# Optimization experiments

Hardware: AMD Instinct MI355X
Metric: run time of the kernel (lower is better)

## Reference

```python
import jax, jax.numpy as jnp
import numpy as np

B, T, N, Fi, Hh, K = 8, 24, 4096, 64, 128, 2
C = Fi + Hh  # concat channel dim


def _uniform(k, shape, fan_in):
    b = 1.0 / np.sqrt(fan_in)
    return jax.random.uniform(k, shape, jnp.float32, -b, b)


def setup_inputs() -> dict:
    key = jax.random.key(0)
    ks = jax.random.split(key, 7)
    x = jax.random.normal(ks[0], (B, T, N, Fi), jnp.float32)
    # torch Conv2d default init: U(-1/sqrt(fan_in), 1/sqrt(fan_in)), fan_in = C_in*kh*kw
    gate_w = _uniform(ks[1], (2 * Hh, C, K, 1), C * K)
    gate_b = _uniform(ks[2], (2 * Hh,), C * K)
    cand_w = _uniform(ks[3], (Hh, C, K, 1), C * K)
    cand_b = _uniform(ks[4], (Hh,), C * K)
    out_w = _uniform(ks[5], (Fi, Hh, 1, 1), Hh)
    out_b = _uniform(ks[6], (Fi,), Hh)
    return {"x": x, "gate_w": gate_w, "gate_b": gate_b,
            "cand_w": cand_w, "cand_b": cand_b,
            "out_w": out_w, "out_b": out_b}


def reference(x, gate_w, gate_b, cand_w, cand_b, out_w, out_b):
    # Conv2d with kernel (K,1), padding (K-1,0) on a height-1 input, keeping only
    # output row 0: out[0] = W[:, :, K-1] @ in[0] (+ zero-padded rows). So each
    # conv reduces to a per-node channel matmul with kernel row K-1.
    Wg = gate_w[:, :, K - 1, 0]  # [2H, C]
    Wc = cand_w[:, :, K - 1, 0]  # [H, C]
    Wo = out_w[:, :, 0, 0]       # [Fi, H]

    def step(h, x_t):
        # h: [B, H, N], x_t: [B, N, Fi]
        xt = jnp.swapaxes(x_t, 1, 2)                       # [B, Fi, N]
        inp = jnp.concatenate([xt, h], axis=1)             # [B, C, N]
        gates = jnp.einsum('bcn,oc->bon', inp, Wg) + gate_b[None, :, None]
        r, z = jnp.split(jax.nn.sigmoid(gates), 2, axis=1)  # each [B, H, N]
        cinp = jnp.concatenate([xt, r * h], axis=1)        # [B, C, N]
        h_tilde = jnp.tanh(jnp.einsum('bcn,oc->bon', cinp, Wc) + cand_b[None, :, None])
        h_t = (1.0 - z) * h + z * h_tilde
        return h_t, h_t

    h0 = jnp.zeros((B, Hh, N), x.dtype)
    _, hs = jax.lax.scan(step, h0, jnp.swapaxes(x, 0, 1))  # hs: [T, B, H, N]
    h_stack = jnp.transpose(hs, (1, 2, 0, 3))              # [B, H, T, N]
    out = jnp.einsum('bhtn,oh->botn', h_stack, Wo) + out_b[None, :, None, None]
    return jax.nn.relu(jnp.transpose(out, (0, 2, 3, 1)))   # [B, T, N, Fi]
```

## Files before the change

kernel.cpp:

```cpp
#include <hip/hip_runtime.h>

#define B_ 8
#define T_ 24
#define N_ 4096
#define FI 64
#define HH 128
#define CC 192
#define COLS 64
#define SI 200
#define SC 136

typedef __bf16 bf16_t;
typedef bf16_t bf16x8 __attribute__((ext_vector_type(8)));
typedef bf16_t bf16x4 __attribute__((ext_vector_type(4)));
typedef float  f32x4  __attribute__((ext_vector_type(4)));

static __device__ __forceinline__ f32x4 mfma16(bf16x8 a, bf16x8 b, f32x4 c) {
    return __builtin_amdgcn_mfma_f32_16x16x32_bf16(a, b, c, 0, 0, 0);
}

__global__ __launch_bounds__(512, 2) void mgru_kernel(
    const float* __restrict__ x,
    const float* __restrict__ gate_w,
    const float* __restrict__ gate_b,
    const float* __restrict__ cand_w,
    const float* __restrict__ cand_b,
    const float* __restrict__ out_w,
    const float* __restrict__ out_b,
    float* __restrict__ out)
{
    __shared__ __align__(16) bf16_t inpT[COLS * SI];
    __shared__ __align__(16) bf16_t cinpT[COLS * SC];

    const int tid  = threadIdx.x;
    const int wave = tid >> 6;
    const int lane = tid & 63;
    const int quad = lane >> 4;
    const int l16  = lane & 15;

    const int bb = blockIdx.x >> 6;
    const int n0 = (blockIdx.x & 63) * COLS;

    for (int i = tid; i < COLS * HH; i += 512) {
        const int col = i >> 7, ch = i & (HH - 1);
        inpT[col * SI + FI + ch] = (bf16_t)0.0f;
    }

    bf16x8 gA[2][6];
    #pragma unroll
    for (int p = 0; p < 2; ++p) {
        const int m = p * 128 + wave * 16 + l16;
        #pragma unroll
        for (int kt = 0; kt < 6; ++kt) {
            bf16x8 f;
            #pragma unroll
            for (int j = 0; j < 8; ++j)
                f[j] = (bf16_t)gate_w[(m * CC + kt * 32 + quad * 8 + j) * 2 + 1];
            gA[p][kt] = f;
        }
    }
    bf16x8 cA[6];
    {
        const int m = wave * 16 + l16;
        #pragma unroll
        for (int kt = 0; kt < 6; ++kt) {
            bf16x8 f;
            #pragma unroll
            for (int j = 0; j < 8; ++j)
                f[j] = (bf16_t)cand_w[(m * CC + kt * 32 + quad * 8 + j) * 2 + 1];
            cA[kt] = f;
        }
    }
    bf16x8 oA[4];
    {
        const int m = (wave >> 1) * 16 + l16;
        #pragma unroll
        for (int kt = 0; kt < 4; ++kt) {
            bf16x8 f;
            #pragma unroll
            for (int j = 0; j < 8; ++j)
                f[j] = (bf16_t)out_w[m * HH + kt * 32 + quad * 8 + j];
            oA[kt] = f;
        }
    }

    f32x4 gBr, gBz, cB, oB;
    #pragma unroll
    for (int r = 0; r < 4; ++r) {
        gBr[r] = gate_b[wave * 16 + quad * 4 + r];
        gBz[r] = gate_b[128 + wave * 16 + quad * 4 + r];
        cB[r]  = cand_b[wave * 16 + quad * 4 + r];
        oB[r]  = out_b[(wave >> 1) * 16 + quad * 4 + r];
    }

    f32x4 hreg[4];
    #pragma unroll
    for (int nt = 0; nt < 4; ++nt) hreg[nt] = f32x4{0.f, 0.f, 0.f, 0.f};

    const int xcol = tid >> 3;
    const int xcg  = (tid & 7) * 8;
    const float* xbase = x   + ((size_t)bb * T_ * N_ + n0) * FI;
    float*       obase = out + ((size_t)bb * T_ * N_ + n0) * FI;

    f32x4 p0 = *(const f32x4*)(xbase + xcol * FI + xcg);
    f32x4 p1 = *(const f32x4*)(xbase + xcol * FI + xcg + 4);

    for (int t = 0; t < T_; ++t) {
        {
            bf16x8 xv;
            xv[0] = (bf16_t)p0[0]; xv[1] = (bf16_t)p0[1];
            xv[2] = (bf16_t)p0[2]; xv[3] = (bf16_t)p0[3];
            xv[4] = (bf16_t)p1[0]; xv[5] = (bf16_t)p1[1];
            xv[6] = (bf16_t)p1[2]; xv[7] = (bf16_t)p1[3];
            *(bf16x8*)&inpT[xcol * SI + xcg] = xv;
        }
        {
            const int tn = (t + 1 < T_) ? t + 1 : t;
            const float* xp = xbase + (size_t)tn * N_ * FI + xcol * FI + xcg;
            p0 = *(const f32x4*)xp;
            p1 = *(const f32x4*)(xp + 4);
        }
        __syncthreads();

        f32x4 ar[4], az[4];
        #pragma unroll
        for (int nt = 0; nt < 4; ++nt) { ar[nt] = gBr; az[nt] = gBz; }
        #pragma unroll
        for (int kt = 0; kt < 6; ++kt) {
            const int ko = kt * 32 + quad * 8;
            bf16x8 b[4];
            #pragma unroll
            for (int nt = 0; nt < 4; ++nt)
                b[nt] = *(const bf16x8*)&inpT[(nt * 16 + l16) * SI + ko];
            #pragma unroll
            for (int nt = 0; nt < 4; ++nt) {
                ar[nt] = mfma16(gA[0][kt], b[nt], ar[nt]);
                az[nt] = mfma16(gA[1][kt], b[nt], az[nt]);
            }
        }
        f32x4 zreg[4];
        #pragma unroll
        for (int nt = 0; nt < 4; ++nt) {
            bf16x4 w;
            #pragma unroll
            for (int r = 0; r < 4; ++r) {
                const float rr = 1.0f / (1.0f + __expf(-ar[nt][r]));
                zreg[nt][r]    = 1.0f / (1.0f + __expf(-az[nt][r]));
                w[r] = (bf16_t)(rr * hreg[nt][r]);
            }
            *(bf16x4*)&cinpT[(nt * 16 + l16) * SC + wave * 16 + quad * 4] = w;
        }
        __syncthreads();

        f32x4 cc[4];
        #pragma unroll
        for (int nt = 0; nt < 4; ++nt) cc[nt] = cB;
        #pragma unroll
        for (int kt = 0; kt < 6; ++kt) {
            const int ko = kt * 32 + quad * 8;
            #pragma unroll
            for (int nt = 0; nt < 4; ++nt) {
                bf16x8 b = (kt < 2)
                    ? *(const bf16x8*)&inpT[(nt * 16 + l16) * SI + ko]
                    : *(const bf16x8*)&cinpT[(nt * 16 + l16) * SC + (ko - FI)];
                cc[nt] = mfma16(cA[kt], b, cc[nt]);
            }
        }
        #pragma unroll
        for (int nt = 0; nt < 4; ++nt) {
            bf16x4 hw;
            #pragma unroll
            for (int r = 0; r < 4; ++r) {
                const float v  = cc[nt][r];
                const float e  = __expf(2.0f * v);
                const float ht = 1.0f - 2.0f / (e + 1.0f);
                const float z  = zreg[nt][r];
                const float h  = hreg[nt][r];
                const float hn = h + z * (ht - h);
                hreg[nt][r] = hn;
                hw[r] = (bf16_t)hn;
            }
            *(bf16x4*)&inpT[(nt * 16 + l16) * SI + FI + wave * 16 + quad * 4] = hw;
        }
        __syncthreads();

        {
            f32x4 oa[2];
            oa[0] = oB; oa[1] = oB;
            const int nb = (wave & 1) * 2;
            #pragma unroll
            for (int kt = 0; kt < 4; ++kt) {
                const int ko = FI + kt * 32 + quad * 8;
                bf16x8 b0 = *(const bf16x8*)&inpT[(nb * 16 + l16) * SI + ko];
                bf16x8 b1 = *(const bf16x8*)&inpT[((nb + 1) * 16 + l16) * SI + ko];
                oa[0] = mfma16(oA[kt], b0, oa[0]);
                oa[1] = mfma16(oA[kt], b1, oa[1]);
            }
            #pragma unroll
            for (int j = 0; j < 2; ++j) {
                const int col = (nb + j) * 16 + l16;
                float* op = obase + (size_t)t * N_ * FI + col * FI + (wave >> 1) * 16 + quad * 4;
                f32x4 o;
                #pragma unroll
                for (int r = 0; r < 4; ++r) o[r] = fmaxf(oa[j][r], 0.0f);
                *(f32x4*)op = o;
            }
        }
    }
}

extern "C" void kernel_launch(void* const* d_in, const int* in_sizes, int n_in,
                              void* d_out, int out_size, void* d_ws, size_t ws_size,
                              hipStream_t stream) {
    (void)in_sizes; (void)n_in; (void)d_ws; (void)ws_size; (void)out_size;
    const float* x      = (const float*)d_in[0];
    const float* gate_w = (const float*)d_in[1];
    const float* gate_b = (const float*)d_in[2];
    const float* cand_w = (const float*)d_in[3];
    const float* cand_b = (const float*)d_in[4];
    const float* out_w  = (const float*)d_in[5];
    const float* out_b  = (const float*)d_in[6];
    float* out = (float*)d_out;
    mgru_kernel<<<dim3(B_ * (N_ / COLS)), dim3(512), 0, stream>>>(
        x, gate_w, gate_b, cand_w, cand_b, out_w, out_b, out);
}
```

Measured before the change: 568.4 us.

## Double-buffer x tile in LDS to drop one barrier per timestep, use fast rcp

Splits the shared input tile into a double-buffered x region and a separate h region, so the next timestep's x can be staged mid-iteration. This removes the barrier that used to follow the x store each step. The division in sigmoid/tanh is replaced with the hardware reciprocal approximation, and s_setprio brackets the MFMA loops. The reciprocal slightly reduces numerical accuracy, and shared memory use grows a little.

```diff
diff --git a/kernel.cpp b/kernel.cpp
--- a/kernel.cpp
+++ b/kernel.cpp
@@ -7,8 +7,9 @@
 #define HH 128
 #define CC 192
 #define COLS 64
-#define SI 200
-#define SC 136
+#define SX 72
+#define SH 136
+#define SC2 136
 
 typedef __bf16 bf16_t;
 typedef bf16_t bf16x8 __attribute__((ext_vector_type(8)));
@@ -17,6 +18,9 @@
 
 static __device__ __forceinline__ f32x4 mfma16(bf16x8 a, bf16x8 b, f32x4 c) {
     return __builtin_amdgcn_mfma_f32_16x16x32_bf16(a, b, c, 0, 0, 0);
+}
+static __device__ __forceinline__ float fast_rcp(float v) {
+    return __builtin_amdgcn_rcpf(v);
 }
 
 __global__ __launch_bounds__(512, 2) void mgru_kernel(
@@ -29,8 +33,9 @@
     const float* __restrict__ out_b,
     float* __restrict__ out)
 {
-    __shared__ __align__(16) bf16_t inpT[COLS * SI];
-    __shared__ __align__(16) bf16_t cinpT[COLS * SC];
+    __shared__ __align__(16) bf16_t xT[2][COLS * SX];
+    __shared__ __align__(16) bf16_t hT[COLS * SH];
+    __shared__ __align__(16) bf16_t cT[COLS * SC2];
 
     const int tid  = threadIdx.x;
     const int wave = tid >> 6;
@@ -43,7 +48,7 @@
 
     for (int i = tid; i < COLS * HH; i += 512) {
         const int col = i >> 7, ch = i & (HH - 1);
-        inpT[col * SI + FI + ch] = (bf16_t)0.0f;
+        hT[col * SH + ch] = (bf16_t)0.0f;
     }
 
     bf16x8 gA[2][6];
@@ -104,68 +109,92 @@
 
     f32x4 p0 = *(const f32x4*)(xbase + xcol * FI + xcg);
     f32x4 p1 = *(const f32x4*)(xbase + xcol * FI + xcg + 4);
-
+    {
+        bf16x8 xv;
+        xv[0] = (bf16_t)p0[0]; xv[1] = (bf16_t)p0[1];
+        xv[2] = (bf16_t)p0[2]; xv[3] = (bf16_t)p0[3];
+        xv[4] = (bf16_t)p1[0]; xv[5] = (bf16_t)p1[1];
+        xv[6] = (bf16_t)p1[2]; xv[7] = (bf16_t)p1[3];
+        *(bf16x8*)&xT[0][xcol * SX + xcg] = xv;
+    }
+    {
+        const float* xp = xbase + (size_t)1 * N_ * FI + xcol * FI + xcg;
+        p0 = *(const f32x4*)xp;
+        p1 = *(const f32x4*)(xp + 4);
+    }
+    __syncthreads();
+
+    int buf = 0;
     for (int t = 0; t < T_; ++t) {
+        const bf16_t* __restrict__ xcur = xT[buf];
+
+        f32x4 ar[4], az[4];
+        #pragma unroll
+        for (int nt = 0; nt < 4; ++nt) { ar[nt] = gBr; az[nt] = gBz; }
+        __builtin_amdgcn_s_setprio(1);
+        #pragma unroll
+        for (int kt = 0; kt < 6; ++kt) {
+            const int ko = kt * 32 + quad * 8;
+            bf16x8 b[4];
+            #pragma unroll
+            for (int nt = 0; nt < 4; ++nt)
+                b[nt] = (kt < 2)
+                    ? *(const bf16x8*)&xcur[(nt * 16 + l16) * SX + ko]
+                    : *(const bf16x8*)&hT[(nt * 16 + l16) * SH + (ko - FI)];
+            #pragma unroll
+            for (int nt = 0; nt < 4; ++nt) {
+                ar[nt] = mfma16(gA[0][kt], b[nt], ar[nt]);
+                az[nt] = mfma16(gA[1][kt], b[nt], az[nt]);
+            }
+        }
+        __builtin_amdgcn_s_setprio(0);
+
+        f32x4 zreg[4];
+        #pragma unroll
+        for (int nt = 0; nt < 4; ++nt) {
+            bf16x4 w;
+            #pragma unroll
+            for (int r = 0; r < 4; ++r) {
+                const float rr = fast_rcp(1.0f + __expf(-ar[nt][r]));
+                zreg[nt][r]    = fast_rcp(1.0f + __expf(-az[nt][r]));
+                w[r] = (bf16_t)(rr * hreg[nt][r]);
+            }
+            *(bf16x4*)&cT[(nt * 16 + l16) * SC2 + wave * 16 + quad * 4] = w;
+        }
+        __syncthreads();
+
         {
             bf16x8 xv;
             xv[0] = (bf16_t)p0[0]; xv[1] = (bf16_t)p0[1];
             xv[2] = (bf16_t)p0[2]; xv[3] = (bf16_t)p0[3];
             xv[4] = (bf16_t)p1[0]; xv[5] = (bf16_t)p1[1];
             xv[6] = (bf16_t)p1[2]; xv[7] = (bf16_t)p1[3];
-            *(bf16x8*)&inpT[xcol * SI + xcg] = xv;
+            *(bf16x8*)&xT[buf ^ 1][xcol * SX + xcg] = xv;
         }
         {
-            const int tn = (t + 1 < T_) ? t + 1 : t;
+            const int tn = (t + 2 < T_) ? t + 2 : T_ - 1;
             const float* xp = xbase + (size_t)tn * N_ * FI + xcol * FI + xcg;
             p0 = *(const f32x4*)xp;
             p1 = *(const f32x4*)(xp + 4);
         }
-        __syncthreads();
-
-        f32x4 ar[4], az[4];
-        #pragma unroll
-        for (int nt = 0; nt < 4; ++nt) { ar[nt] = gBr; az[nt] = gBz; }
-        #pragma unroll
-        for (int kt = 0; kt < 6; ++kt) {
-            const int ko = kt * 32 + quad * 8;
-            bf16x8 b[4];
-            #pragma unroll
-            for (int nt = 0; nt < 4; ++nt)
-                b[nt] = *(const bf16x8*)&inpT[(nt * 16 + l16) * SI + ko];
-            #pragma unroll
-            for (int nt = 0; nt < 4; ++nt) {
-                ar[nt] = mfma16(gA[0][kt], b[nt], ar[nt]);
-                az[nt] = mfma16(gA[1][kt], b[nt], az[nt]);
-            }
-        }
-        f32x4 zreg[4];
-        #pragma unroll
-        for (int nt = 0; nt < 4; ++nt) {
-            bf16x4 w;
-            #pragma unroll
-            for (int r = 0; r < 4; ++r) {
-                const float rr = 1.0f / (1.0f + __expf(-ar[nt][r]));
-                zreg[nt][r]    = 1.0f / (1.0f + __expf(-az[nt][r]));
-                w[r] = (bf16_t)(rr * hreg[nt][r]);
-            }
-            *(bf16x4*)&cinpT[(nt * 16 + l16) * SC + wave * 16 + quad * 4] = w;
-        }
-        __syncthreads();
 
         f32x4 cc[4];
         #pragma unroll
         for (int nt = 0; nt < 4; ++nt) cc[nt] = cB;
+        __builtin_amdgcn_s_setprio(1);
         #pragma unroll
         for (int kt = 0; kt < 6; ++kt) {
             const int ko = kt * 32 + quad * 8;
             #pragma unroll
             for (int nt = 0; nt < 4; ++nt) {
                 bf16x8 b = (kt < 2)
-                    ? *(const bf16x8*)&inpT[(nt * 16 + l16) * SI + ko]
-                    : *(const bf16x8*)&cinpT[(nt * 16 + l16) * SC + (ko - FI)];
+                    ? *(const bf16x8*)&xcur[(nt * 16 + l16) * SX + ko]
+                    : *(const bf16x8*)&cT[(nt * 16 + l16) * SC2 + (ko - FI)];
                 cc[nt] = mfma16(cA[kt], b, cc[nt]);
             }
         }
+        __builtin_amdgcn_s_setprio(0);
+
         #pragma unroll
         for (int nt = 0; nt < 4; ++nt) {
             bf16x4 hw;
@@ -173,14 +202,14 @@
             for (int r = 0; r < 4; ++r) {
                 const float v  = cc[nt][r];
                 const float e  = __expf(2.0f * v);
-                const float ht = 1.0f - 2.0f / (e + 1.0f);
+                const float ht = 1.0f - 2.0f * fast_rcp(e + 1.0f);
                 const float z  = zreg[nt][r];
                 const float h  = hreg[nt][r];
                 const float hn = h + z * (ht - h);
                 hreg[nt][r] = hn;
                 hw[r] = (bf16_t)hn;
             }
-            *(bf16x4*)&inpT[(nt * 16 + l16) * SI + FI + wave * 16 + quad * 4] = hw;
+            *(bf16x4*)&hT[(nt * 16 + l16) * SH + wave * 16 + quad * 4] = hw;
         }
         __syncthreads();
 
@@ -188,14 +217,16 @@
             f32x4 oa[2];
             oa[0] = oB; oa[1] = oB;
             const int nb = (wave & 1) * 2;
+            __builtin_amdgcn_s_setprio(1);
             #pragma unroll
             for (int kt = 0; kt < 4; ++kt) {
-                const int ko = FI + kt * 32 + quad * 8;
-                bf16x8 b0 = *(const bf16x8*)&inpT[(nb * 16 + l16) * SI + ko];
-                bf16x8 b1 = *(const bf16x8*)&inpT[((nb + 1) * 16 + l16) * SI + ko];
+                const int ko = kt * 32 + quad * 8;
+                bf16x8 b0 = *(const bf16x8*)&hT[(nb * 16 + l16) * SH + ko];
+                bf16x8 b1 = *(const bf16x8*)&hT[((nb + 1) * 16 + l16) * SH + ko];
                 oa[0] = mfma16(oA[kt], b0, oa[0]);
                 oa[1] = mfma16(oA[kt], b1, oa[1]);
             }
+            __builtin_amdgcn_s_setprio(0);
             #pragma unroll
             for (int j = 0; j < 2; ++j) {
                 const int col = (nb + j) * 16 + l16;
@@ -206,6 +237,7 @@
                 *(f32x4*)op = o;
             }
         }
+        buf ^= 1;
     }
 }
 
```

Measured after the change: 459.9 us. 19.1% less time.
